# Kernel optimization log

Measured on AMD Instinct MI355X. Metric: run time of the kernel, lower is better.

The kernel has to match this reference:

```python
import jax, jax.numpy as jnp
import numpy as np

CUTOFF = 5.0       # module __init__ arg
BOX_L = 40.0       # side of cubic region positions are drawn from (OBC: no box passed)
N_ATOMS = 8192
MAX_PAIRS = 1_048_576  # static bound on directed pairs (expected ~550k)


def setup_inputs() -> dict:
    key = jax.random.key(0)
    positions = jax.random.uniform(key, (N_ATOMS, 3), dtype=jnp.float32) * BOX_L
    return {"positions": positions}


def _pairwise_dist(x):
    # Euclidean distance matrix via the gram trick (avoids [N,N,3] intermediate).
    sq = jnp.sum(x * x, axis=1)
    d2 = sq[:, None] + sq[None, :] - 2.0 * (x @ x.T)
    return jnp.sqrt(jnp.maximum(d2, 0.0))


def _safe_norm(dr):
    # norm with zero-safe gradient (padded pairs have dr == 0)
    d2 = jnp.sum(dr * dr, axis=1)
    ok = d2 > 0
    return jnp.where(ok, jnp.sqrt(jnp.where(ok, d2, 1.0)), 0.0)


def reference(positions):
    n = positions.shape[0]
    dist = _pairwise_dist(positions)                      # [N, N]
    mask = (dist < CUTOFF) & (~jnp.eye(n, dtype=bool))    # exclude self-pairs
    # torch.argwhere equivalent, padded to static size; padding -> (0, 0)
    i, j = jnp.nonzero(mask, size=MAX_PAIRS, fill_value=0)
    pairs = jnp.stack([i, j], axis=1).astype(jnp.int32)   # [MAX_PAIRS, 2]
    # pairs_buffer_scales: 1 where i < j else 0 (padding (0,0) -> 0)
    buffer_scales = (i < j).astype(jnp.int32)
    # pairs_ds (pbc_flag=False): ||r_j - r_i||
    dr = positions[j] - positions[i]                      # [MAX_PAIRS, 3]
    ds = _safe_norm(dr)
    return pairs, buffer_scales, ds
```

## Files before the change

### kernel.cpp

```cpp
#include <hip/hip_runtime.h>

#define MAXP 1048576
#define NATOMS 8192
#define D2_CUT 0x1.8ffffep+4f
#define CINV 0.175f
#define CAP 192

#define W_CELLOFF 0
#define W_SORTID  512
#define W_ROWCNT  8704
#define W_ROWOFF  16896
#define W_SORTPOS 25088

__device__ __forceinline__ float sq3_nc(float x, float y, float z) {
#pragma clang fp contract(off)
  float a = x * x;
  float b = y * y;
  float c = z * z;
  return (a + b) + c;
}

__device__ __forceinline__ float d2_gram(float xi, float yi, float zi, float sqi,
                                         float xj, float yj, float zj, float sqj) {
#pragma clang fp contract(off)
  float g = xi * xj;
  g = __builtin_fmaf(yi, yj, g);
  g = __builtin_fmaf(zi, zj, g);
  float t = sqi + sqj;
  float d2 = t - 2.0f * g;
  return d2;
}

__device__ __forceinline__ float d2_direct(float xi, float yi, float zi,
                                           float xj, float yj, float zj) {
#pragma clang fp contract(off)
  float dx = xj - xi;
  float dy = yj - yi;
  float dz = zj - zi;
  float a = dx * dx;
  float b = dy * dy;
  float c = dz * dz;
  return (a + b) + c;
}

__device__ __forceinline__ int cellco(float v) {
  int c = (int)(v * CINV);
  return c < 0 ? 0 : (c > 6 ? 6 : c);
}

__global__ __launch_bounds__(1024) void nl_prep(const float* __restrict__ pos,
                                                float* __restrict__ ws) {
  __shared__ int hcnt[343];
  __shared__ int hoff[344];
  __shared__ int hcur[343];
  __shared__ int s[512];
  const int tid = threadIdx.x;
  if (tid < 343) { hcnt[tid] = 0; hcur[tid] = 0; }
  __syncthreads();

  float x[8], y[8], z[8];
  int cl[8];
#pragma unroll
  for (int k = 0; k < 8; ++k) {
    int a = tid + k * 1024;
    x[k] = pos[3 * a]; y[k] = pos[3 * a + 1]; z[k] = pos[3 * a + 2];
    cl[k] = cellco(x[k]) + 7 * cellco(y[k]) + 49 * cellco(z[k]);
    atomicAdd(&hcnt[cl[k]], 1);
  }
  __syncthreads();

  if (tid < 512) s[tid] = (tid < 343) ? hcnt[tid] : 0;
  __syncthreads();
  for (int off = 1; off < 512; off <<= 1) {
    int v = (tid < 512 && tid >= off) ? s[tid - off] : 0;
    __syncthreads();
    if (tid < 512) s[tid] += v;
    __syncthreads();
  }
  if (tid < 343) hoff[tid] = (tid == 0) ? 0 : s[tid - 1];
  if (tid == 343) hoff[343] = NATOMS;
  __syncthreads();
  if (tid < 344) ((int*)(ws + W_CELLOFF))[tid] = hoff[tid];

  int* sortid = (int*)(ws + W_SORTID);
  float4* sortpos = (float4*)(ws + W_SORTPOS);
#pragma unroll
  for (int k = 0; k < 8; ++k) {
    int slot = hoff[cl[k]] + atomicAdd(&hcur[cl[k]], 1);
    sortid[slot] = tid + k * 1024;
    sortpos[slot] = make_float4(x[k], y[k], z[k], sq3_nc(x[k], y[k], z[k]));
  }
}

__global__ __launch_bounds__(256) void nl_rowcount(const float* __restrict__ pos,
                                                   float* __restrict__ out,
                                                   float* __restrict__ ws) {
  float4* o4 = (float4*)out;
  const int b = blockIdx.x;
  o4[b * 512 + threadIdx.x] = make_float4(0.f, 0.f, 0.f, 0.f);
  o4[b * 512 + 256 + threadIdx.x] = make_float4(0.f, 0.f, 0.f, 0.f);

  const int* celloff = (const int*)(ws + W_CELLOFF);
  const int* sortid = (const int*)(ws + W_SORTID);
  const float4* sortpos = (const float4*)(ws + W_SORTPOS);
  int* rowcnt = (int*)(ws + W_ROWCNT);
  const int lane = threadIdx.x & 63;
  const int wave = threadIdx.x >> 6;
  const int row = b * 4 + wave;
  float xi = pos[3 * row], yi = pos[3 * row + 1], zi = pos[3 * row + 2];
  float sqi = sq3_nc(xi, yi, zi);
  int cx = cellco(xi), cy = cellco(yi), cz = cellco(zi);
  int x0 = max(cx - 1, 0), x1 = min(cx + 1, 6);
  int y0 = max(cy - 1, 0), y1 = min(cy + 1, 6);
  int z0 = max(cz - 1, 0), z1 = min(cz + 1, 6);
  int cnt = 0;
  for (int icz = z0; icz <= z1; ++icz)
    for (int icy = y0; icy <= y1; ++icy) {
      int cb = 7 * icy + 49 * icz;
      int st = celloff[cb + x0];
      int en = celloff[cb + x1 + 1];
      for (int bb = st; bb < en; bb += 64) {
        int t = bb + lane;
        bool v = t < en;
        float4 p = v ? sortpos[t] : make_float4(1e30f, 1e30f, 1e30f, 0.f);
        int j = v ? sortid[t] : -1;
        float d2 = d2_gram(xi, yi, zi, sqi, p.x, p.y, p.z, p.w);
        cnt += (v && (d2 < D2_CUT) && (j != row)) ? 1 : 0;
      }
    }
  for (int off = 32; off > 0; off >>= 1) cnt += __shfl_down(cnt, off, 64);
  if (lane == 0) rowcnt[row] = cnt;
}

__global__ __launch_bounds__(1024) void nl_rowscan(float* __restrict__ ws) {
  const int* cnts = (const int*)(ws + W_ROWCNT);
  int* offs = (int*)(ws + W_ROWOFF);
  __shared__ int s[1024];
  const int tid = threadIdx.x;
  const int base = tid * 8;
  int local[8];
  int sum = 0;
#pragma unroll
  for (int k = 0; k < 8; ++k) { local[k] = sum; sum += cnts[base + k]; }
  s[tid] = sum;
  __syncthreads();
  for (int off = 1; off < 1024; off <<= 1) {
    int v = (tid >= off) ? s[tid - off] : 0;
    __syncthreads();
    s[tid] += v;
    __syncthreads();
  }
  int excl = (tid == 0) ? 0 : s[tid - 1];
#pragma unroll
  for (int k = 0; k < 8; ++k) offs[base + k] = excl + local[k];
}

__global__ __launch_bounds__(256) void nl_rowwrite(const float* __restrict__ pos,
                                                   float* __restrict__ out,
                                                   const float* __restrict__ ws) {
  const int* celloff = (const int*)(ws + W_CELLOFF);
  const int* sortid = (const int*)(ws + W_SORTID);
  const float4* sortpos = (const float4*)(ws + W_SORTPOS);
  const int* rowoff = (const int*)(ws + W_ROWOFF);
  __shared__ int jb[4][CAP];
  __shared__ float db[4][CAP];
  const int lane = threadIdx.x & 63;
  const int wave = threadIdx.x >> 6;
  const int row = blockIdx.x * 4 + wave;
  float xi = pos[3 * row], yi = pos[3 * row + 1], zi = pos[3 * row + 2];
  float sqi = sq3_nc(xi, yi, zi);
  int cx = cellco(xi), cy = cellco(yi), cz = cellco(zi);
  int x0 = max(cx - 1, 0), x1 = min(cx + 1, 6);
  int y0 = max(cy - 1, 0), y1 = min(cy + 1, 6);
  int z0 = max(cz - 1, 0), z1 = min(cz + 1, 6);
  int cnt = 0;
  for (int icz = z0; icz <= z1; ++icz)
    for (int icy = y0; icy <= y1; ++icy) {
      int cb = 7 * icy + 49 * icz;
      int st = celloff[cb + x0];
      int en = celloff[cb + x1 + 1];
      for (int bb = st; bb < en; bb += 64) {
        int t = bb + lane;
        bool v = t < en;
        float4 p = v ? sortpos[t] : make_float4(1e30f, 1e30f, 1e30f, 0.f);
        int j = v ? sortid[t] : -1;
        float d2 = d2_gram(xi, yi, zi, sqi, p.x, p.y, p.z, p.w);
        bool pred = v && (d2 < D2_CUT) && (j != row);
        unsigned long long m = __ballot(pred ? 1 : 0);
        if (pred) {
          int ps = cnt + __popcll(m & ((1ull << lane) - 1ull));
          if (ps < CAP) {
            jb[wave][ps] = j;
            db[wave][ps] = sqrtf(d2_direct(xi, yi, zi, p.x, p.y, p.z));
          }
        }
        cnt += __popcll(m);
      }
    }
  int k = cnt > CAP ? CAP : cnt;
  int base = rowoff[row];
  for (int midx = lane; midx < k; midx += 64) {
    int jm = jb[wave][midx];
    int rank = 0;
    for (int t = 0; t < k; ++t) rank += (jb[wave][t] < jm) ? 1 : 0;
    int idx = base + rank;
    if (idx < MAXP) {
      ((float2*)out)[idx] = make_float2((float)row, (float)jm);
      out[2 * MAXP + idx] = (row < jm) ? 1.0f : 0.0f;
      out[3 * MAXP + idx] = db[wave][midx];
    }
  }
}

extern "C" void kernel_launch(void* const* d_in, const int* in_sizes, int n_in,
                              void* d_out, int out_size, void* d_ws, size_t ws_size,
                              hipStream_t stream) {
  const float* pos = (const float*)d_in[0];
  float* out = (float*)d_out;
  float* ws = (float*)d_ws;

  nl_prep<<<1, 1024, 0, stream>>>(pos, ws);
  nl_rowcount<<<NATOMS / 4, 256, 0, stream>>>(pos, out, ws);
  nl_rowscan<<<1, 1024, 0, stream>>>(ws);
  nl_rowwrite<<<NATOMS / 4, 256, 0, stream>>>(pos, out, ws);
}
```

Before: 101.1 us.

## Replace cell-list neighbor search with brute-force all-pairs tiled scan

Drops the single-block cell binning and sort kernel. Count and write kernels now scan all 8192 atoms in 64-wide tiles, with each wave handling 8 rows so each loaded position is reused across those rows. Pairs are emitted directly in column order via ballot/popcount, which removes the shared-memory buffer and the O(k^2) rank sort. This trades about 25x more distance evaluations for no serial prep kernel, no cell bookkeeping and no per-row sort. Output zeroing moves into a separate pack kernel.

```diff
diff --git a/kernel.cpp b/kernel.cpp
--- a/kernel.cpp
+++ b/kernel.cpp
@@ -3,14 +3,10 @@
 #define MAXP 1048576
 #define NATOMS 8192
 #define D2_CUT 0x1.8ffffep+4f
-#define CINV 0.175f
-#define CAP 192
 
-#define W_CELLOFF 0
-#define W_SORTID  512
-#define W_ROWCNT  8704
-#define W_ROWOFF  16896
-#define W_SORTPOS 25088
+#define W_P4     0
+#define W_ROWCNT 32768
+#define W_ROWOFF 40960
 
 __device__ __forceinline__ float sq3_nc(float x, float y, float z) {
 #pragma clang fp contract(off)
@@ -43,93 +39,58 @@
   return (a + b) + c;
 }
 
-__device__ __forceinline__ int cellco(float v) {
-  int c = (int)(v * CINV);
-  return c < 0 ? 0 : (c > 6 ? 6 : c);
-}
-
-__global__ __launch_bounds__(1024) void nl_prep(const float* __restrict__ pos,
-                                                float* __restrict__ ws) {
-  __shared__ int hcnt[343];
-  __shared__ int hoff[344];
-  __shared__ int hcur[343];
-  __shared__ int s[512];
-  const int tid = threadIdx.x;
-  if (tid < 343) { hcnt[tid] = 0; hcur[tid] = 0; }
-  __syncthreads();
-
-  float x[8], y[8], z[8];
-  int cl[8];
+__global__ __launch_bounds__(256) void nl_pack(const float* __restrict__ pos,
+                                               float* __restrict__ out,
+                                               float* __restrict__ ws) {
+  const int gtid = blockIdx.x * 256 + threadIdx.x;
+  float4* o4 = (float4*)out;
 #pragma unroll
-  for (int k = 0; k < 8; ++k) {
-    int a = tid + k * 1024;
-    x[k] = pos[3 * a]; y[k] = pos[3 * a + 1]; z[k] = pos[3 * a + 2];
-    cl[k] = cellco(x[k]) + 7 * cellco(y[k]) + 49 * cellco(z[k]);
-    atomicAdd(&hcnt[cl[k]], 1);
-  }
-  __syncthreads();
-
-  if (tid < 512) s[tid] = (tid < 343) ? hcnt[tid] : 0;
-  __syncthreads();
-  for (int off = 1; off < 512; off <<= 1) {
-    int v = (tid < 512 && tid >= off) ? s[tid - off] : 0;
-    __syncthreads();
-    if (tid < 512) s[tid] += v;
-    __syncthreads();
-  }
-  if (tid < 343) hoff[tid] = (tid == 0) ? 0 : s[tid - 1];
-  if (tid == 343) hoff[343] = NATOMS;
-  __syncthreads();
-  if (tid < 344) ((int*)(ws + W_CELLOFF))[tid] = hoff[tid];
-
-  int* sortid = (int*)(ws + W_SORTID);
-  float4* sortpos = (float4*)(ws + W_SORTPOS);
-#pragma unroll
-  for (int k = 0; k < 8; ++k) {
-    int slot = hoff[cl[k]] + atomicAdd(&hcur[cl[k]], 1);
-    sortid[slot] = tid + k * 1024;
-    sortpos[slot] = make_float4(x[k], y[k], z[k], sq3_nc(x[k], y[k], z[k]));
+  for (int k = 0; k < 16; ++k)
+    o4[k * 65536 + gtid] = make_float4(0.f, 0.f, 0.f, 0.f);
+  if (gtid < NATOMS) {
+    float x = pos[3 * gtid], y = pos[3 * gtid + 1], z = pos[3 * gtid + 2];
+    ((float4*)(ws + W_P4))[gtid] = make_float4(x, y, z, sq3_nc(x, y, z));
   }
 }
 
-__global__ __launch_bounds__(256) void nl_rowcount(const float* __restrict__ pos,
-                                                   float* __restrict__ out,
-                                                   float* __restrict__ ws) {
-  float4* o4 = (float4*)out;
-  const int b = blockIdx.x;
-  o4[b * 512 + threadIdx.x] = make_float4(0.f, 0.f, 0.f, 0.f);
-  o4[b * 512 + 256 + threadIdx.x] = make_float4(0.f, 0.f, 0.f, 0.f);
+__global__ __launch_bounds__(256) void nl_count(const float* __restrict__ pos,
+                                                float* __restrict__ ws) {
+  const int tid = threadIdx.x;
+  const int lane = tid & 63;
+  const int wave = tid >> 6;
+  const int rowbase = (blockIdx.x * 4 + wave) * 8;
 
-  const int* celloff = (const int*)(ws + W_CELLOFF);
-  const int* sortid = (const int*)(ws + W_SORTID);
-  const float4* sortpos = (const float4*)(ws + W_SORTPOS);
+  const float4* __restrict__ p4 = (const float4*)(ws + W_P4);
   int* rowcnt = (int*)(ws + W_ROWCNT);
-  const int lane = threadIdx.x & 63;
-  const int wave = threadIdx.x >> 6;
-  const int row = b * 4 + wave;
-  float xi = pos[3 * row], yi = pos[3 * row + 1], zi = pos[3 * row + 2];
-  float sqi = sq3_nc(xi, yi, zi);
-  int cx = cellco(xi), cy = cellco(yi), cz = cellco(zi);
-  int x0 = max(cx - 1, 0), x1 = min(cx + 1, 6);
-  int y0 = max(cy - 1, 0), y1 = min(cy + 1, 6);
-  int z0 = max(cz - 1, 0), z1 = min(cz + 1, 6);
-  int cnt = 0;
-  for (int icz = z0; icz <= z1; ++icz)
-    for (int icy = y0; icy <= y1; ++icy) {
-      int cb = 7 * icy + 49 * icz;
-      int st = celloff[cb + x0];
-      int en = celloff[cb + x1 + 1];
-      for (int bb = st; bb < en; bb += 64) {
-        int t = bb + lane;
-        bool v = t < en;
-        float4 p = v ? sortpos[t] : make_float4(1e30f, 1e30f, 1e30f, 0.f);
-        int j = v ? sortid[t] : -1;
-        float d2 = d2_gram(xi, yi, zi, sqi, p.x, p.y, p.z, p.w);
-        cnt += (v && (d2 < D2_CUT) && (j != row)) ? 1 : 0;
-      }
+
+  float xi[8], yi[8], zi[8], sqi[8];
+#pragma unroll
+  for (int r = 0; r < 8; ++r) {
+    int row = rowbase + r;
+    xi[r] = pos[3 * row];
+    yi[r] = pos[3 * row + 1];
+    zi[r] = pos[3 * row + 2];
+    sqi[r] = sq3_nc(xi[r], yi[r], zi[r]);
+  }
+
+  int cnt[8] = {0, 0, 0, 0, 0, 0, 0, 0};
+  const int selfTile = rowbase >> 6;
+
+#pragma unroll 4
+  for (int t = 0; t < 128; ++t) {
+    float4 p = p4[t * 64 + lane];
+#pragma unroll
+    for (int r = 0; r < 8; ++r) {
+      float d2 = d2_gram(xi[r], yi[r], zi[r], sqi[r], p.x, p.y, p.z, p.w);
+      unsigned long long m = __ballot((d2 < D2_CUT) ? 1 : 0);
+      if (t == selfTile) m &= ~(1ull << ((rowbase & 63) + r));
+      cnt[r] += __popcll(m);
     }
-  for (int off = 32; off > 0; off >>= 1) cnt += __shfl_down(cnt, off, 64);
-  if (lane == 0) rowcnt[row] = cnt;
+  }
+  if (lane == 0) {
+#pragma unroll
+    for (int r = 0; r < 8; ++r) rowcnt[rowbase + r] = cnt[r];
+  }
 }
 
 __global__ __launch_bounds__(1024) void nl_rowscan(float* __restrict__ ws) {
@@ -155,59 +116,53 @@
   for (int k = 0; k < 8; ++k) offs[base + k] = excl + local[k];
 }
 
-__global__ __launch_bounds__(256) void nl_rowwrite(const float* __restrict__ pos,
-                                                   float* __restrict__ out,
-                                                   const float* __restrict__ ws) {
-  const int* celloff = (const int*)(ws + W_CELLOFF);
-  const int* sortid = (const int*)(ws + W_SORTID);
-  const float4* sortpos = (const float4*)(ws + W_SORTPOS);
+__global__ __launch_bounds__(256) void nl_write(const float* __restrict__ pos,
+                                               float* __restrict__ out,
+                                               const float* __restrict__ ws) {
+  const int tid = threadIdx.x;
+  const int lane = tid & 63;
+  const int wave = tid >> 6;
+  const int rowbase = (blockIdx.x * 4 + wave) * 8;
+
+  const float4* __restrict__ p4 = (const float4*)(ws + W_P4);
   const int* rowoff = (const int*)(ws + W_ROWOFF);
-  __shared__ int jb[4][CAP];
-  __shared__ float db[4][CAP];
-  const int lane = threadIdx.x & 63;
-  const int wave = threadIdx.x >> 6;
-  const int row = blockIdx.x * 4 + wave;
-  float xi = pos[3 * row], yi = pos[3 * row + 1], zi = pos[3 * row + 2];
-  float sqi = sq3_nc(xi, yi, zi);
-  int cx = cellco(xi), cy = cellco(yi), cz = cellco(zi);
-  int x0 = max(cx - 1, 0), x1 = min(cx + 1, 6);
-  int y0 = max(cy - 1, 0), y1 = min(cy + 1, 6);
-  int z0 = max(cz - 1, 0), z1 = min(cz + 1, 6);
-  int cnt = 0;
-  for (int icz = z0; icz <= z1; ++icz)
-    for (int icy = y0; icy <= y1; ++icy) {
-      int cb = 7 * icy + 49 * icz;
-      int st = celloff[cb + x0];
-      int en = celloff[cb + x1 + 1];
-      for (int bb = st; bb < en; bb += 64) {
-        int t = bb + lane;
-        bool v = t < en;
-        float4 p = v ? sortpos[t] : make_float4(1e30f, 1e30f, 1e30f, 0.f);
-        int j = v ? sortid[t] : -1;
-        float d2 = d2_gram(xi, yi, zi, sqi, p.x, p.y, p.z, p.w);
-        bool pred = v && (d2 < D2_CUT) && (j != row);
-        unsigned long long m = __ballot(pred ? 1 : 0);
-        if (pred) {
-          int ps = cnt + __popcll(m & ((1ull << lane) - 1ull));
-          if (ps < CAP) {
-            jb[wave][ps] = j;
-            db[wave][ps] = sqrtf(d2_direct(xi, yi, zi, p.x, p.y, p.z));
-          }
+
+  float xi[8], yi[8], zi[8], sqi[8];
+  int base[8];
+#pragma unroll
+  for (int r = 0; r < 8; ++r) {
+    int row = rowbase + r;
+    xi[r] = pos[3 * row];
+    yi[r] = pos[3 * row + 1];
+    zi[r] = pos[3 * row + 2];
+    sqi[r] = sq3_nc(xi[r], yi[r], zi[r]);
+    base[r] = rowoff[row];
+  }
+
+  int cnt[8] = {0, 0, 0, 0, 0, 0, 0, 0};
+  const int selfTile = rowbase >> 6;
+  const unsigned long long lmask = (1ull << lane) - 1ull;
+
+  for (int t = 0; t < 128; ++t) {
+    float4 p = p4[t * 64 + lane];
+    const int j = t * 64 + lane;
+#pragma unroll
+    for (int r = 0; r < 8; ++r) {
+      const int row = rowbase + r;
+      float d2 = d2_gram(xi[r], yi[r], zi[r], sqi[r], p.x, p.y, p.z, p.w);
+      bool pred = d2 < D2_CUT;
+      unsigned long long m = __ballot(pred ? 1 : 0);
+      if (t == selfTile) m &= ~(1ull << ((rowbase & 63) + r));
+      if (pred && j != row) {
+        int o = base[r] + cnt[r] + __popcll(m & lmask);
+        if ((unsigned)o < MAXP) {
+          float ds = sqrtf(d2_direct(xi[r], yi[r], zi[r], p.x, p.y, p.z));
+          ((float2*)out)[o] = make_float2((float)row, (float)j);
+          out[2 * MAXP + o] = (row < j) ? 1.0f : 0.0f;
+          out[3 * MAXP + o] = ds;
         }
-        cnt += __popcll(m);
       }
-    }
-  int k = cnt > CAP ? CAP : cnt;
-  int base = rowoff[row];
-  for (int midx = lane; midx < k; midx += 64) {
-    int jm = jb[wave][midx];
-    int rank = 0;
-    for (int t = 0; t < k; ++t) rank += (jb[wave][t] < jm) ? 1 : 0;
-    int idx = base + rank;
-    if (idx < MAXP) {
-      ((float2*)out)[idx] = make_float2((float)row, (float)jm);
-      out[2 * MAXP + idx] = (row < jm) ? 1.0f : 0.0f;
-      out[3 * MAXP + idx] = db[wave][midx];
+      cnt[r] += __popcll(m);
     }
   }
 }
@@ -219,8 +174,8 @@
   float* out = (float*)d_out;
   float* ws = (float*)d_ws;
 
-  nl_prep<<<1, 1024, 0, stream>>>(pos, ws);
-  nl_rowcount<<<NATOMS / 4, 256, 0, stream>>>(pos, out, ws);
+  nl_pack<<<256, 256, 0, stream>>>(pos, out, ws);
+  nl_count<<<256, 256, 0, stream>>>(pos, ws);
   nl_rowscan<<<1, 1024, 0, stream>>>(ws);
-  nl_rowwrite<<<NATOMS / 4, 256, 0, stream>>>(pos, out, ws);
+  nl_write<<<256, 256, 0, stream>>>(pos, out, ws);
 }
```

Result: slower. 216.1 us (+113.8%).

## Split cell binning into multi-block kernels and sort neighbors via shared bitmap

Applied to the files above, without the earlier changes.

Replaces the single-block prep kernel with separate multi-block cell-count, scan and scatter kernels, and moves output zeroing into its own grid-wide kernel. The write kernel now marks neighbors in a per-row shared-memory bitmap with atomicOr and emits them in index order by popcount prefix, replacing the quadratic rank sort. Distances are recomputed from original positions at write time. Self-exclusion moves to a count-minus-one and a bitmap clear, and sort ids are stored as 16-bit. This adds four kernel launches and relies on row counts staying under CAP.

```diff
diff --git a/kernel.cpp b/kernel.cpp
--- a/kernel.cpp
+++ b/kernel.cpp
@@ -6,11 +6,13 @@
 #define CINV 0.175f
 #define CAP 192
 
-#define W_CELLOFF 0
-#define W_SORTID  512
-#define W_ROWCNT  8704
-#define W_ROWOFF  16896
-#define W_SORTPOS 25088
+#define W_SORTPOS 0
+#define W_SORTID  32768
+#define W_ROWCNT  36864
+#define W_ROWOFF  45056
+#define W_CELLOFF 53248
+#define W_CELLCNT 53760
+#define W_CELLCUR 54272
 
 __device__ __forceinline__ float sq3_nc(float x, float y, float z) {
 #pragma clang fp contract(off)
@@ -48,71 +50,70 @@
   return c < 0 ? 0 : (c > 6 ? 6 : c);
 }
 
-__global__ __launch_bounds__(1024) void nl_prep(const float* __restrict__ pos,
-                                                float* __restrict__ ws) {
-  __shared__ int hcnt[343];
-  __shared__ int hoff[344];
-  __shared__ int hcur[343];
+__global__ __launch_bounds__(256) void nl_pack(float* __restrict__ out,
+                                               float* __restrict__ ws) {
+  const int gtid = blockIdx.x * 256 + threadIdx.x;
+  float4* o4 = (float4*)out;
+#pragma unroll
+  for (int k = 0; k < 16; ++k)
+    o4[k * 65536 + gtid] = make_float4(0.f, 0.f, 0.f, 0.f);
+  if (gtid < 512) ((int*)(ws + W_CELLCNT))[gtid] = 0;
+}
+
+__global__ __launch_bounds__(256) void nl_cellcount(const float* __restrict__ pos,
+                                                    float* __restrict__ ws) {
+  const int a = blockIdx.x * 256 + threadIdx.x;
+  float x = pos[3 * a], y = pos[3 * a + 1], z = pos[3 * a + 2];
+  int cl = cellco(x) + 7 * cellco(y) + 49 * cellco(z);
+  atomicAdd(&((int*)(ws + W_CELLCNT))[cl], 1);
+}
+
+__global__ __launch_bounds__(512) void nl_cellscan(float* __restrict__ ws) {
+  const int* cellcnt = (const int*)(ws + W_CELLCNT);
+  int* celloff = (int*)(ws + W_CELLOFF);
+  int* cellcur = (int*)(ws + W_CELLCUR);
   __shared__ int s[512];
   const int tid = threadIdx.x;
-  if (tid < 343) { hcnt[tid] = 0; hcur[tid] = 0; }
-  __syncthreads();
-
-  float x[8], y[8], z[8];
-  int cl[8];
-#pragma unroll
-  for (int k = 0; k < 8; ++k) {
-    int a = tid + k * 1024;
-    x[k] = pos[3 * a]; y[k] = pos[3 * a + 1]; z[k] = pos[3 * a + 2];
-    cl[k] = cellco(x[k]) + 7 * cellco(y[k]) + 49 * cellco(z[k]);
-    atomicAdd(&hcnt[cl[k]], 1);
-  }
-  __syncthreads();
-
-  if (tid < 512) s[tid] = (tid < 343) ? hcnt[tid] : 0;
+  s[tid] = (tid < 343) ? cellcnt[tid] : 0;
   __syncthreads();
   for (int off = 1; off < 512; off <<= 1) {
-    int v = (tid < 512 && tid >= off) ? s[tid - off] : 0;
-    __syncthreads();
-    if (tid < 512) s[tid] += v;
-    __syncthreads();
-  }
-  if (tid < 343) hoff[tid] = (tid == 0) ? 0 : s[tid - 1];
-  if (tid == 343) hoff[343] = NATOMS;
-  __syncthreads();
-  if (tid < 344) ((int*)(ws + W_CELLOFF))[tid] = hoff[tid];
-
-  int* sortid = (int*)(ws + W_SORTID);
-  float4* sortpos = (float4*)(ws + W_SORTPOS);
-#pragma unroll
-  for (int k = 0; k < 8; ++k) {
-    int slot = hoff[cl[k]] + atomicAdd(&hcur[cl[k]], 1);
-    sortid[slot] = tid + k * 1024;
-    sortpos[slot] = make_float4(x[k], y[k], z[k], sq3_nc(x[k], y[k], z[k]));
-  }
-}
-
-__global__ __launch_bounds__(256) void nl_rowcount(const float* __restrict__ pos,
-                                                   float* __restrict__ out,
+    int v = (tid >= off) ? s[tid - off] : 0;
+    __syncthreads();
+    s[tid] += v;
+    __syncthreads();
+  }
+  if (tid < 344) celloff[tid] = (tid == 0) ? 0 : s[tid - 1];
+  cellcur[tid] = 0;
+}
+
+__global__ __launch_bounds__(256) void nl_scatter(const float* __restrict__ pos,
+                                                  float* __restrict__ ws) {
+  const int a = blockIdx.x * 256 + threadIdx.x;
+  float x = pos[3 * a], y = pos[3 * a + 1], z = pos[3 * a + 2];
+  int cl = cellco(x) + 7 * cellco(y) + 49 * cellco(z);
+  int slot = ((const int*)(ws + W_CELLOFF))[cl] +
+             atomicAdd(&((int*)(ws + W_CELLCUR))[cl], 1);
+  ((float4*)(ws + W_SORTPOS))[slot] = make_float4(x, y, z, sq3_nc(x, y, z));
+  ((unsigned short*)(ws + W_SORTID))[slot] = (unsigned short)a;
+}
+
+__global__ __launch_bounds__(256, 4) void nl_count(const float* __restrict__ pos,
                                                    float* __restrict__ ws) {
-  float4* o4 = (float4*)out;
-  const int b = blockIdx.x;
-  o4[b * 512 + threadIdx.x] = make_float4(0.f, 0.f, 0.f, 0.f);
-  o4[b * 512 + 256 + threadIdx.x] = make_float4(0.f, 0.f, 0.f, 0.f);
-
-  const int* celloff = (const int*)(ws + W_CELLOFF);
-  const int* sortid = (const int*)(ws + W_SORTID);
-  const float4* sortpos = (const float4*)(ws + W_SORTPOS);
-  int* rowcnt = (int*)(ws + W_ROWCNT);
   const int lane = threadIdx.x & 63;
   const int wave = threadIdx.x >> 6;
-  const int row = b * 4 + wave;
-  float xi = pos[3 * row], yi = pos[3 * row + 1], zi = pos[3 * row + 2];
-  float sqi = sq3_nc(xi, yi, zi);
+  const int row = blockIdx.x * 4 + wave;
+
+  const float4* __restrict__ sp4 = (const float4*)(ws + W_SORTPOS);
+  const int* __restrict__ celloff = (const int*)(ws + W_CELLOFF);
+  int* rowcnt = (int*)(ws + W_ROWCNT);
+
+  const float xi = pos[3 * row], yi = pos[3 * row + 1], zi = pos[3 * row + 2];
+  const float sqi = sq3_nc(xi, yi, zi);
   int cx = cellco(xi), cy = cellco(yi), cz = cellco(zi);
   int x0 = max(cx - 1, 0), x1 = min(cx + 1, 6);
   int y0 = max(cy - 1, 0), y1 = min(cy + 1, 6);
   int z0 = max(cz - 1, 0), z1 = min(cz + 1, 6);
+
   int cnt = 0;
   for (int icz = z0; icz <= z1; ++icz)
     for (int icy = y0; icy <= y1; ++icy) {
@@ -122,14 +123,14 @@
       for (int bb = st; bb < en; bb += 64) {
         int t = bb + lane;
         bool v = t < en;
-        float4 p = v ? sortpos[t] : make_float4(1e30f, 1e30f, 1e30f, 0.f);
-        int j = v ? sortid[t] : -1;
+        int t2 = v ? t : (en - 1);
+        float4 p = sp4[t2];
         float d2 = d2_gram(xi, yi, zi, sqi, p.x, p.y, p.z, p.w);
-        cnt += (v && (d2 < D2_CUT) && (j != row)) ? 1 : 0;
+        cnt += (v && d2 < D2_CUT) ? 1 : 0;
       }
     }
   for (int off = 32; off > 0; off >>= 1) cnt += __shfl_down(cnt, off, 64);
-  if (lane == 0) rowcnt[row] = cnt;
+  if (lane == 0) rowcnt[row] = cnt - 1;
 }
 
 __global__ __launch_bounds__(1024) void nl_rowscan(float* __restrict__ ws) {
@@ -155,25 +156,30 @@
   for (int k = 0; k < 8; ++k) offs[base + k] = excl + local[k];
 }
 
-__global__ __launch_bounds__(256) void nl_rowwrite(const float* __restrict__ pos,
+__global__ __launch_bounds__(256, 4) void nl_write(const float* __restrict__ pos,
                                                    float* __restrict__ out,
                                                    const float* __restrict__ ws) {
-  const int* celloff = (const int*)(ws + W_CELLOFF);
-  const int* sortid = (const int*)(ws + W_SORTID);
-  const float4* sortpos = (const float4*)(ws + W_SORTPOS);
-  const int* rowoff = (const int*)(ws + W_ROWOFF);
-  __shared__ int jb[4][CAP];
-  __shared__ float db[4][CAP];
+  __shared__ unsigned int bmap[4][256];
+  __shared__ unsigned short stj[4][CAP];
   const int lane = threadIdx.x & 63;
   const int wave = threadIdx.x >> 6;
   const int row = blockIdx.x * 4 + wave;
-  float xi = pos[3 * row], yi = pos[3 * row + 1], zi = pos[3 * row + 2];
-  float sqi = sq3_nc(xi, yi, zi);
+
+  const float4* __restrict__ sp4 = (const float4*)(ws + W_SORTPOS);
+  const unsigned short* __restrict__ sid = (const unsigned short*)(ws + W_SORTID);
+  const int* __restrict__ celloff = (const int*)(ws + W_CELLOFF);
+  const int* __restrict__ rowoff = (const int*)(ws + W_ROWOFF);
+
+#pragma unroll
+  for (int q = 0; q < 4; ++q) bmap[wave][lane + 64 * q] = 0u;
+
+  const float xi = pos[3 * row], yi = pos[3 * row + 1], zi = pos[3 * row + 2];
+  const float sqi = sq3_nc(xi, yi, zi);
   int cx = cellco(xi), cy = cellco(yi), cz = cellco(zi);
   int x0 = max(cx - 1, 0), x1 = min(cx + 1, 6);
   int y0 = max(cy - 1, 0), y1 = min(cy + 1, 6);
   int z0 = max(cz - 1, 0), z1 = min(cz + 1, 6);
-  int cnt = 0;
+
   for (int icz = z0; icz <= z1; ++icz)
     for (int icy = y0; icy <= y1; ++icy) {
       int cb = 7 * icy + 49 * icz;
@@ -182,32 +188,49 @@
       for (int bb = st; bb < en; bb += 64) {
         int t = bb + lane;
         bool v = t < en;
-        float4 p = v ? sortpos[t] : make_float4(1e30f, 1e30f, 1e30f, 0.f);
-        int j = v ? sortid[t] : -1;
+        int t2 = v ? t : (en - 1);
+        float4 p = sp4[t2];
+        int jd = sid[t2];
         float d2 = d2_gram(xi, yi, zi, sqi, p.x, p.y, p.z, p.w);
-        bool pred = v && (d2 < D2_CUT) && (j != row);
-        unsigned long long m = __ballot(pred ? 1 : 0);
-        if (pred) {
-          int ps = cnt + __popcll(m & ((1ull << lane) - 1ull));
-          if (ps < CAP) {
-            jb[wave][ps] = j;
-            db[wave][ps] = sqrtf(d2_direct(xi, yi, zi, p.x, p.y, p.z));
-          }
-        }
-        cnt += __popcll(m);
+        if (v && d2 < D2_CUT)
+          atomicOr(&bmap[wave][jd >> 5], 1u << (jd & 31));
       }
     }
-  int k = cnt > CAP ? CAP : cnt;
-  int base = rowoff[row];
-  for (int midx = lane; midx < k; midx += 64) {
-    int jm = jb[wave][midx];
-    int rank = 0;
-    for (int t = 0; t < k; ++t) rank += (jb[wave][t] < jm) ? 1 : 0;
-    int idx = base + rank;
-    if (idx < MAXP) {
-      ((float2*)out)[idx] = make_float2((float)row, (float)jm);
-      out[2 * MAXP + idx] = (row < jm) ? 1.0f : 0.0f;
-      out[3 * MAXP + idx] = db[wave][midx];
+  if (lane == 0)
+    atomicAnd(&bmap[wave][row >> 5], ~(1u << (row & 31)));
+
+  int ktot = 0;
+#pragma unroll
+  for (int seg = 0; seg < 4; ++seg) {
+    int w = seg * 64 + lane;
+    unsigned bits = bmap[wave][w];
+    int pc = __popc(bits);
+    int incl = pc;
+    for (int d = 1; d < 64; d <<= 1) {
+      int u = __shfl_up(incl, d, 64);
+      if (lane >= d) incl += u;
+    }
+    int base = ktot + incl - pc;
+    while (bits) {
+      int b = __builtin_ctz(bits);
+      bits &= bits - 1;
+      if (base < CAP) stj[wave][base] = (unsigned short)(w * 32 + b);
+      ++base;
+    }
+    ktot += __shfl(incl, 63, 64);
+  }
+
+  int k = ktot > CAP ? CAP : ktot;
+  int ro = rowoff[row];
+  for (int s = lane; s < k; s += 64) {
+    int j = stj[wave][s];
+    int o = ro + s;
+    if ((unsigned)o < MAXP) {
+      float xj = pos[3 * j], yj = pos[3 * j + 1], zj = pos[3 * j + 2];
+      float ds = sqrtf(d2_direct(xi, yi, zi, xj, yj, zj));
+      ((float2*)out)[o] = make_float2((float)row, (float)j);
+      out[2 * MAXP + o] = (row < j) ? 1.0f : 0.0f;
+      out[3 * MAXP + o] = ds;
     }
   }
 }
@@ -219,8 +242,11 @@
   float* out = (float*)d_out;
   float* ws = (float*)d_ws;
 
-  nl_prep<<<1, 1024, 0, stream>>>(pos, ws);
-  nl_rowcount<<<NATOMS / 4, 256, 0, stream>>>(pos, out, ws);
+  nl_pack<<<256, 256, 0, stream>>>(out, ws);
+  nl_cellcount<<<32, 256, 0, stream>>>(pos, ws);
+  nl_cellscan<<<1, 512, 0, stream>>>(ws);
+  nl_scatter<<<32, 256, 0, stream>>>(pos, ws);
+  nl_count<<<2048, 256, 0, stream>>>(pos, ws);
   nl_rowscan<<<1, 1024, 0, stream>>>(ws);
-  nl_rowwrite<<<NATOMS / 4, 256, 0, stream>>>(pos, out, ws);
-}
+  nl_write<<<2048, 256, 0, stream>>>(pos, out, ws);
+}
```

Result: faster. 96.04 us (-5.0%).
